# Optimization experiments

Hardware: AMD Instinct MI355X
Metric: run time of the kernel (lower is better)

Reference implementation:

```python
import jax, jax.numpy as jnp
import numpy as np

B, N, IN_DIM, HID = 16, 2048, 128, 128
EPS = 1e-5


def _layer(x, W, b, g, beta):
    # x: (B, N, d_in) -> (B, N, HID)
    h = jnp.einsum('bnd,dh->bnh', x, W) + b
    mu = jnp.mean(h, axis=-1, keepdims=True)
    var = jnp.mean((h - mu) ** 2, axis=-1, keepdims=True)
    h = (h - mu) * jax.lax.rsqrt(var + EPS) * g + beta
    return jax.nn.relu(h)


def setup_inputs() -> dict:
    key = jax.random.key(0)
    ks = jax.random.split(key, 8)
    x = jax.random.normal(ks[0], (B, N, IN_DIM), dtype=jnp.float32)
    adj = jax.random.uniform(ks[1], (B, N, N), dtype=jnp.float32)
    inp = {'x': x, 'adj': adj}
    dims = [IN_DIM, HID, HID]
    for i in range(3):
        d_in = dims[i]
        scale = 1.0 / np.sqrt(d_in)
        inp[f'W{i}'] = jax.random.uniform(ks[2 + i], (d_in, HID), dtype=jnp.float32, minval=-scale, maxval=scale)
        inp[f'b{i}'] = jax.random.uniform(ks[5 + i], (HID,), dtype=jnp.float32, minval=-scale, maxval=scale)
        inp[f'g{i}'] = jnp.ones((HID,), dtype=jnp.float32)
        inp[f'be{i}'] = jnp.zeros((HID,), dtype=jnp.float32)
    return inp


def reference(x, adj, W0, b0, g0, be0, W1, b1, g1, be1, W2, b2, g2, be2):
    params = [(W0, b0, g0, be0), (W1, b1, g1, be1), (W2, b2, g2, be2)]
    h = x
    for (W, b, g, beta) in params:
        h_agg = jnp.einsum('bnm,bmd->bnd', adj, h)  # dense adjacency aggregation
        h = _layer(h_agg, W, b, g, beta)
    return h
```

## Files before the change

### kernel.cpp

```cpp
#include <hip/hip_runtime.h>
#include <hip/hip_bf16.h>

typedef __bf16 bf16;
typedef __bf16 bf16x8 __attribute__((ext_vector_type(8)));
typedef float  f32x4  __attribute__((ext_vector_type(4)));

static constexpr int NB  = 16;
static constexpr int NN  = 2048;
static constexpr int HID = 128;

__device__ __forceinline__ void gload_lds16(const bf16* g, bf16* l) {
    __builtin_amdgcn_global_load_lds(
        (const __attribute__((address_space(1))) unsigned int*)g,
        (__attribute__((address_space(3))) unsigned int*)l, 16, 0, 0);
}
__device__ __forceinline__ void memfence() { asm volatile("" ::: "memory"); }


__global__ __launch_bounds__(256) void prep_wt(const float* __restrict__ W0,
                                               const float* __restrict__ W1,
                                               const float* __restrict__ W2,
                                               bf16* __restrict__ WTg) {
    int l = blockIdx.x;
    const float* W = (l == 0) ? W0 : (l == 1) ? W1 : W2;
    bf16* out = WTg + l * 16384;
    int tid = threadIdx.x;
#pragma unroll
    for (int i = 0; i < 8; ++i) {
        int p = i * 256 + tid;
        int n = p >> 4, half = (p >> 3) & 1, cs = p & 7;
        int kc = cs ^ (n & 7);
        int kbase = half * 64 + kc * 8;
        bf16x8 o;
#pragma unroll
        for (int r = 0; r < 8; ++r) o[r] = (bf16)W[(kbase + r) * 128 + n];
        *(bf16x8*)(out + p * 8) = o;
    }
}

__global__ __launch_bounds__(256) void prep_xt(const float* __restrict__ x,
                                               bf16* __restrict__ xTt) {
    __shared__ bf16 T[128 * 136];
    const int blk = blockIdx.x;
    const int b = blk >> 4, node0 = (blk & 15) * 128;
    const int tid = threadIdx.x;
    const float* xb = x + ((size_t)b * NN + node0) * HID;
#pragma unroll
    for (int i = 0; i < 64; ++i) {
        int idx = i * 256 + tid;
        int node = idx >> 7, hid = idx & 127;
        T[hid * 136 + node] = (bf16)xb[(size_t)node * HID + hid];
    }
    __syncthreads();
#pragma unroll
    for (int i = 0; i < 8; ++i) {
        int p = i * 256 + tid;
        int half = p >> 10, p1 = p & 1023;
        int n = p1 >> 3, cs = p1 & 7, c = cs ^ (n & 7), m = half * 64 + c * 8;
        *(bf16x8*)(xTt + ((size_t)b * 32 + (node0 >> 6) + half) * 8192 + p1 * 8)
            = *(const bf16x8*)(T + n * 136 + m);
    }
}

template<int AMODE, bool FINAL>
__global__ __launch_bounds__(512, 2) void fused_layer(
        const float* __restrict__ Af, bf16* __restrict__ adjT,
        const bf16* __restrict__ Bt, const bf16* __restrict__ WTg,
        const float* __restrict__ bias, const float* __restrict__ gam,
        const float* __restrict__ bet, bf16* __restrict__ hOut,
        float* __restrict__ outF) {
    __shared__ __align__(16) bf16 lds[49152];
    bf16* WTl = lds + 32768;

    const int tid = threadIdx.x, wave = tid >> 6, lane = tid & 63;
    const int c0 = lane & 15, q = lane >> 4;
    const int blk = blockIdx.x, xcd = blk & 7, jj = blk >> 3;
    const int b = xcd * 2 + (jj & 1);
    const int mtile = jj >> 1, m0 = mtile * 128;
    const int wm = wave >> 1, wn = wave & 1;

    const bf16* Btb = Bt + (size_t)b * 32 * 8192;
    bf16* Atl = adjT + ((size_t)b * 16 + mtile) * 32 * 8192;

    f32x4 acc[2][4] = {};

#pragma unroll
    for (int j = 0; j < 4; ++j) {
        int cb = j * 512 + wave * 64;
        gload_lds16(WTg + (size_t)(cb + lane) * 8, WTl + cb * 8);
    }

    auto stageA2 = [&](int buf, int kk) {
#pragma unroll
        for (int j = 0; j < 2; ++j) {
            int cb = j * 512 + wave * 64;
            gload_lds16(Atl + (size_t)kk * 8192 + (size_t)(cb + lane) * 8,
                        lds + buf * 16384 + cb * 8);
        }
    };
    auto stageB2 = [&](int buf, int kk) {
#pragma unroll
        for (int j = 0; j < 2; ++j) {
            int cb = j * 512 + wave * 64;
            gload_lds16(Btb + (size_t)kk * 8192 + (size_t)(cb + lane) * 8,
                        lds + buf * 16384 + 8192 + cb * 8);
        }
    };
    auto compute = [&](int buf) {
        const bf16* As = lds + buf * 16384;
        const bf16* Bs = As + 8192;
#pragma unroll
        for (int ks = 0; ks < 2; ++ks) {
            bf16x8 af[2], bf_[4];
#pragma unroll
            for (int mt = 0; mt < 2; ++mt) {
                int row = wm * 32 + mt * 16 + c0;
                int cb = (ks * 4 + q) ^ (row & 7);
                af[mt] = *(const bf16x8*)(As + row * 64 + cb * 8);
            }
#pragma unroll
            for (int nt = 0; nt < 4; ++nt) {
                int row = wn * 64 + nt * 16 + c0;
                int cb = (ks * 4 + q) ^ (row & 7);
                bf_[nt] = *(const bf16x8*)(Bs + row * 64 + cb * 8);
            }
#pragma unroll
            for (int mt = 0; mt < 2; ++mt)
#pragma unroll
                for (int nt = 0; nt < 4; ++nt)
                    acc[mt][nt] = __builtin_amdgcn_mfma_f32_16x16x32_bf16(
                        af[mt], bf_[nt], acc[mt][nt], 0, 0, 0);
        }
    };

    if constexpr (AMODE == 1) {
        int grow[2], gcb[2];
#pragma unroll
        for (int j = 0; j < 2; ++j) {
            int gi = j * 512 + tid;
            grow[j] = gi >> 3; gcb[j] = gi & 7;
        }
        f32x4 va[2], vb[2];
        auto loadA = [&](int kk) {
#pragma unroll
            for (int j = 0; j < 2; ++j) {
                const float* s = Af + (size_t)b * NN * NN
                               + (size_t)(m0 + grow[j]) * NN + kk * 64 + gcb[j] * 8;
                va[j] = *(const f32x4*)s;
                vb[j] = *(const f32x4*)(s + 4);
            }
        };
        auto writeA = [&](int buf, int kk) {
#pragma unroll
            for (int j = 0; j < 2; ++j) {
                bf16x8 o = {(bf16)va[j].x, (bf16)va[j].y, (bf16)va[j].z, (bf16)va[j].w,
                            (bf16)vb[j].x, (bf16)vb[j].y, (bf16)vb[j].z, (bf16)vb[j].w};
                int ch = grow[j] * 8 + (gcb[j] ^ (grow[j] & 7));
                *(bf16x8*)(lds + buf * 16384 + ch * 8) = o;
                *(bf16x8*)(Atl + (size_t)kk * 8192 + ch * 8) = o;
            }
        };
        loadA(0); stageB2(0, 0); writeA(0, 0);
        __syncthreads();
        int cur = 0;
        for (int kk = 0; kk < 32; ++kk) {
            if (kk < 31) { loadA(kk + 1); stageB2(cur ^ 1, kk + 1); }
            compute(cur);
            if (kk < 31) writeA(cur ^ 1, kk + 1);
            __syncthreads();
            cur ^= 1;
        }
    } else {
        stageA2(0, 0); stageB2(0, 0);
        stageA2(1, 1); stageB2(1, 1);
#pragma unroll 1
        for (int kk = 0; kk < 32; ++kk) {
            if (kk < 31) asm volatile("s_waitcnt vmcnt(4)" ::: "memory");
            else         asm volatile("s_waitcnt vmcnt(0)" ::: "memory");
            __builtin_amdgcn_s_barrier();
            memfence();
            compute(kk & 1);
            memfence();
            __builtin_amdgcn_s_barrier();
            if (kk < 30) { stageA2(kk & 1, kk + 2); stageB2(kk & 1, kk + 2); }
        }
        __syncthreads();
    }

    bf16* G = lds;
#pragma unroll
    for (int mt = 0; mt < 2; ++mt)
#pragma unroll
        for (int r = 0; r < 4; ++r) {
            int row = wm * 32 + mt * 16 + q * 4 + r;
#pragma unroll
            for (int nt = 0; nt < 4; ++nt) {
                int col = wn * 64 + nt * 16 + c0;
                G[row * 136 + col] = (bf16)acc[mt][nt][r];
            }
        }
    __syncthreads();

    f32x4 a2[8] = {};
    {
        const int gr = wave * 16 + c0;
#pragma unroll
        for (int ks = 0; ks < 4; ++ks) {
            bf16x8 af = *(const bf16x8*)(G + gr * 136 + ks * 32 + q * 8);
#pragma unroll
            for (int nt = 0; nt < 8; ++nt) {
                int n = nt * 16 + c0;
                int ch = n * 16 + (ks >> 1) * 8 + ((((ks & 1) << 2) | q) ^ (n & 7));
                bf16x8 bw = *(const bf16x8*)(WTl + ch * 8);
                a2[nt] = __builtin_amdgcn_mfma_f32_16x16x32_bf16(af, bw, a2[nt], 0, 0, 0);
            }
        }
    }

    float bv[8], gv[8], ev[8];
#pragma unroll
    for (int nt = 0; nt < 8; ++nt) {
        int n = nt * 16 + c0;
        bv[nt] = bias[n]; gv[nt] = gam[n]; ev[nt] = bet[n];
    }
    bf16* Cs = lds;
    if constexpr (!FINAL) __syncthreads();
#pragma unroll
    for (int r = 0; r < 4; ++r) {
        float v[8], s1 = 0.f, s2 = 0.f;
#pragma unroll
        for (int nt = 0; nt < 8; ++nt) {
            float xv = a2[nt][r] + bv[nt];
            v[nt] = xv; s1 += xv; s2 += xv * xv;
        }
#pragma unroll
        for (int off = 1; off < 16; off <<= 1) {
            s1 += __shfl_xor(s1, off);
            s2 += __shfl_xor(s2, off);
        }
        float mu = s1 * (1.f / 128.f);
        float var = s2 * (1.f / 128.f) - mu * mu;
        float rs = rsqrtf(var + 1e-5f);
        int row = wave * 16 + q * 4 + r;
        if constexpr (FINAL) {
            size_t ro = ((size_t)b * NN + m0 + row) * HID;
#pragma unroll
            for (int nt = 0; nt < 8; ++nt) {
                float o = fmaxf((v[nt] - mu) * rs * gv[nt] + ev[nt], 0.f);
                outF[ro + nt * 16 + c0] = o;
            }
        } else {
#pragma unroll
            for (int nt = 0; nt < 8; ++nt) {
                float o = fmaxf((v[nt] - mu) * rs * gv[nt] + ev[nt], 0.f);
                Cs[(nt * 16 + c0) * 136 + row] = (bf16)o;
            }
        }
    }
    if constexpr (!FINAL) {
        __syncthreads();
#pragma unroll
        for (int i = 0; i < 4; ++i) {
            int p = i * 512 + tid;
            int half = p >> 10, p1 = p & 1023;
            int n = p1 >> 3, cs = p1 & 7, c = cs ^ (n & 7), m = half * 64 + c * 8;
            *(bf16x8*)(hOut + ((size_t)b * 32 + mtile * 2 + half) * 8192 + p1 * 8)
                = *(const bf16x8*)(Cs + n * 136 + m);
        }
    }
}

extern "C" void kernel_launch(void* const* d_in, const int* in_sizes, int n_in,
                              void* d_out, int out_size, void* d_ws, size_t ws_size,
                              hipStream_t stream) {
    const float* x   = (const float*)d_in[0];
    const float* adj = (const float*)d_in[1];
    const float* W[3]  = {(const float*)d_in[2],  (const float*)d_in[6],  (const float*)d_in[10]};
    const float* bb[3] = {(const float*)d_in[3],  (const float*)d_in[7],  (const float*)d_in[11]};
    const float* gg[3] = {(const float*)d_in[4],  (const float*)d_in[8],  (const float*)d_in[12]};
    const float* be[3] = {(const float*)d_in[5],  (const float*)d_in[9],  (const float*)d_in[13]};

    char* ws = (char*)d_ws;
    size_t off = 0;
    auto alloc = [&](size_t bytes) {
        char* p = ws + off; off = (off + bytes + 255) & ~(size_t)255; return p;
    };
    bf16* WTg  = (bf16*)alloc((size_t)3 * 16384 * 2);
    bf16* xTt  = (bf16*)alloc((size_t)NB * 32 * 8192 * 2);
    bf16* hT0  = (bf16*)alloc((size_t)NB * 32 * 8192 * 2);
    bf16* hT1  = (bf16*)alloc((size_t)NB * 32 * 8192 * 2);
    bf16* adjT = (bf16*)alloc((size_t)NB * 16 * 32 * 8192 * 2);

    float* outF = (float*)d_out;

    prep_wt<<<3, 256, 0, stream>>>(W[0], W[1], W[2], WTg);
    prep_xt<<<256, 256, 0, stream>>>(x, xTt);

    fused_layer<1, false><<<256, 512, 0, stream>>>(adj, adjT, xTt, WTg,
                                                   bb[0], gg[0], be[0], hT0, nullptr);
    fused_layer<2, false><<<256, 512, 0, stream>>>(adj, adjT, hT0, WTg + 16384,
                                                   bb[1], gg[1], be[1], hT1, nullptr);
    fused_layer<2, true ><<<256, 512, 0, stream>>>(adj, adjT, hT1, WTg + 2 * 16384,
                                                   bb[2], gg[2], be[2], nullptr, outF);
}
```

Measured before the change: 494.7 us.

## Retile fused GNN layer to 64-row blocks with 4-stage register-fed A pipeline

Changes the fused aggregation+linear+layernorm kernel from 128-row tiles with 512 threads to 64-row tiles with 256 threads and 512 blocks. Each wave now loads its own adjacency rows straight into registers (fp32 converted in-register on layer 1, bf16 cache reused after that) instead of staging A through LDS. The B tiles are staged through a 4-deep LDS ring with vmcnt-based waits and a single barrier per step. The goal is better latency hiding on the memory-bound adjacency stream, more blocks resident per CU, and no LDS traffic for A. The cost is a changed adjT layout, more register pressure, and W being loaded late into LDS after the main loop.

```diff
diff --git a/kernel.cpp b/kernel.cpp
--- a/kernel.cpp
+++ b/kernel.cpp
@@ -14,7 +14,8 @@
         (const __attribute__((address_space(1))) unsigned int*)g,
         (__attribute__((address_space(3))) unsigned int*)l, 16, 0, 0);
 }
-__device__ __forceinline__ void memfence() { asm volatile("" ::: "memory"); }
+
+#define WAITV(n) asm volatile("s_waitcnt vmcnt(" #n ")" ::: "memory")
 
 
 __global__ __launch_bounds__(256) void prep_wt(const float* __restrict__ W0,
@@ -63,142 +64,124 @@
 }
 
 template<int AMODE, bool FINAL>
-__global__ __launch_bounds__(512, 2) void fused_layer(
+__global__ __launch_bounds__(256, 2) void fused64(
         const float* __restrict__ Af, bf16* __restrict__ adjT,
         const bf16* __restrict__ Bt, const bf16* __restrict__ WTg,
         const float* __restrict__ bias, const float* __restrict__ gam,
         const float* __restrict__ bet, bf16* __restrict__ hOut,
         float* __restrict__ outF) {
-    __shared__ __align__(16) bf16 lds[49152];
-    bf16* WTl = lds + 32768;
+    __shared__ __align__(16) bf16 lds[32768];
 
     const int tid = threadIdx.x, wave = tid >> 6, lane = tid & 63;
     const int c0 = lane & 15, q = lane >> 4;
     const int blk = blockIdx.x, xcd = blk & 7, jj = blk >> 3;
     const int b = xcd * 2 + (jj & 1);
-    const int mtile = jj >> 1, m0 = mtile * 128;
-    const int wm = wave >> 1, wn = wave & 1;
+    const int mt = jj >> 1, m0 = mt * 64;
 
     const bf16* Btb = Bt + (size_t)b * 32 * 8192;
-    bf16* Atl = adjT + ((size_t)b * 16 + mtile) * 32 * 8192;
-
-    f32x4 acc[2][4] = {};
-
-#pragma unroll
-    for (int j = 0; j < 4; ++j) {
-        int cb = j * 512 + wave * 64;
-        gload_lds16(WTg + (size_t)(cb + lane) * 8, WTl + cb * 8);
-    }
-
-    auto stageA2 = [&](int buf, int kk) {
-#pragma unroll
-        for (int j = 0; j < 2; ++j) {
-            int cb = j * 512 + wave * 64;
-            gload_lds16(Atl + (size_t)kk * 8192 + (size_t)(cb + lane) * 8,
-                        lds + buf * 16384 + cb * 8);
-        }
-    };
-    auto stageB2 = [&](int buf, int kk) {
-#pragma unroll
-        for (int j = 0; j < 2; ++j) {
-            int cb = j * 512 + wave * 64;
-            gload_lds16(Btb + (size_t)kk * 8192 + (size_t)(cb + lane) * 8,
-                        lds + buf * 16384 + 8192 + cb * 8);
-        }
-    };
-    auto compute = [&](int buf) {
-        const bf16* As = lds + buf * 16384;
-        const bf16* Bs = As + 8192;
-#pragma unroll
-        for (int ks = 0; ks < 2; ++ks) {
-            bf16x8 af[2], bf_[4];
-#pragma unroll
-            for (int mt = 0; mt < 2; ++mt) {
-                int row = wm * 32 + mt * 16 + c0;
-                int cb = (ks * 4 + q) ^ (row & 7);
-                af[mt] = *(const bf16x8*)(As + row * 64 + cb * 8);
-            }
-#pragma unroll
-            for (int nt = 0; nt < 4; ++nt) {
-                int row = wn * 64 + nt * 16 + c0;
-                int cb = (ks * 4 + q) ^ (row & 7);
-                bf_[nt] = *(const bf16x8*)(Bs + row * 64 + cb * 8);
-            }
-#pragma unroll
-            for (int mt = 0; mt < 2; ++mt)
-#pragma unroll
-                for (int nt = 0; nt < 4; ++nt)
-                    acc[mt][nt] = __builtin_amdgcn_mfma_f32_16x16x32_bf16(
-                        af[mt], bf_[nt], acc[mt][nt], 0, 0, 0);
-        }
-    };
-
-    if constexpr (AMODE == 1) {
-        int grow[2], gcb[2];
-#pragma unroll
-        for (int j = 0; j < 2; ++j) {
-            int gi = j * 512 + tid;
-            grow[j] = gi >> 3; gcb[j] = gi & 7;
-        }
-        f32x4 va[2], vb[2];
-        auto loadA = [&](int kk) {
-#pragma unroll
-            for (int j = 0; j < 2; ++j) {
-                const float* s = Af + (size_t)b * NN * NN
-                               + (size_t)(m0 + grow[j]) * NN + kk * 64 + gcb[j] * 8;
-                va[j] = *(const f32x4*)s;
-                vb[j] = *(const f32x4*)(s + 4);
-            }
-        };
-        auto writeA = [&](int buf, int kk) {
-#pragma unroll
-            for (int j = 0; j < 2; ++j) {
-                bf16x8 o = {(bf16)va[j].x, (bf16)va[j].y, (bf16)va[j].z, (bf16)va[j].w,
-                            (bf16)vb[j].x, (bf16)vb[j].y, (bf16)vb[j].z, (bf16)vb[j].w};
-                int ch = grow[j] * 8 + (gcb[j] ^ (grow[j] & 7));
-                *(bf16x8*)(lds + buf * 16384 + ch * 8) = o;
-                *(bf16x8*)(Atl + (size_t)kk * 8192 + ch * 8) = o;
-            }
-        };
-        loadA(0); stageB2(0, 0); writeA(0, 0);
-        __syncthreads();
-        int cur = 0;
-        for (int kk = 0; kk < 32; ++kk) {
-            if (kk < 31) { loadA(kk + 1); stageB2(cur ^ 1, kk + 1); }
-            compute(cur);
-            if (kk < 31) writeA(cur ^ 1, kk + 1);
-            __syncthreads();
-            cur ^= 1;
-        }
-    } else {
-        stageA2(0, 0); stageB2(0, 0);
-        stageA2(1, 1); stageB2(1, 1);
+    bf16* Atl = adjT + ((size_t)b * 32 + mt) * (size_t)32 * 4096;
+    const float* Aln = Af + (size_t)b * NN * NN
+                     + (size_t)(m0 + wave * 16 + c0) * NN + q * 8;
+    const int fofs = wave * 128 + lane;
+
+    f32x4 acc[8] = {};
+    bf16x8 aA[4][2];
+    f32x4  aF[4][2][2];
+
+#define LOADA(S, KK) do {                                                     \
+    if constexpr (AMODE == 1) {                                               \
+        _Pragma("unroll") for (int ks = 0; ks < 2; ++ks) {                    \
+            const float* s_ = Aln + (KK) * 64 + ks * 32;                      \
+            aF[S][ks][0] = *(const f32x4*)s_;                                 \
+            aF[S][ks][1] = *(const f32x4*)(s_ + 4);                           \
+        }                                                                     \
+    } else {                                                                  \
+        _Pragma("unroll") for (int ks = 0; ks < 2; ++ks)                      \
+            aA[S][ks] = *(const bf16x8*)(Atl + (size_t)(KK) * 4096            \
+                                         + (fofs + ks * 64) * 8);             \
+    } } while (0)
+
+#define STAGEB(S, KK) do {                                                    \
+    _Pragma("unroll") for (int j = 0; j < 4; ++j) {                           \
+        int cb = j * 256 + wave * 64;                                         \
+        gload_lds16(Btb + (size_t)(KK) * 8192 + (size_t)(cb + lane) * 8,      \
+                    lds + (S) * 8192 + cb * 8);                               \
+    } } while (0)
+
+#define COMP(S, KK) do {                                                      \
+    bf16x8 af_[2];                                                            \
+    if constexpr (AMODE == 1) {                                               \
+        _Pragma("unroll") for (int ks = 0; ks < 2; ++ks) {                    \
+            f32x4 lo = aF[S][ks][0], hi = aF[S][ks][1];                       \
+            bf16x8 o = {(bf16)lo.x, (bf16)lo.y, (bf16)lo.z, (bf16)lo.w,       \
+                        (bf16)hi.x, (bf16)hi.y, (bf16)hi.z, (bf16)hi.w};      \
+            af_[ks] = o;                                                      \
+            *(bf16x8*)(Atl + (size_t)(KK) * 4096 + (fofs + ks * 64) * 8) = o; \
+        }                                                                     \
+    } else { af_[0] = aA[S][0]; af_[1] = aA[S][1]; }                          \
+    const bf16* Bs_ = lds + (S) * 8192;                                       \
+    _Pragma("unroll") for (int ks = 0; ks < 2; ++ks)                          \
+        _Pragma("unroll") for (int nt = 0; nt < 8; ++nt) {                    \
+            int row = nt * 16 + c0, cb = (ks * 4 + q) ^ (row & 7);            \
+            bf16x8 bw = *(const bf16x8*)(Bs_ + row * 64 + cb * 8);            \
+            acc[nt] = __builtin_amdgcn_mfma_f32_16x16x32_bf16(                \
+                af_[ks], bw, acc[nt], 0, 0, 0);                               \
+        } } while (0)
+
+    LOADA(0, 0); STAGEB(0, 0);
+    LOADA(1, 1); STAGEB(1, 1);
+    LOADA(2, 2); STAGEB(2, 2);
+
+#define ITERU(U, KB)                                                          \
+    { if constexpr (AMODE == 1) WAITV(20); else WAITV(12);                    \
+      __builtin_amdgcn_s_barrier();                                           \
+      COMP(U, (KB) + (U));                                                    \
+      LOADA(((U) + 3) & 3, (KB) + (U) + 3);                                   \
+      STAGEB(((U) + 3) & 3, (KB) + (U) + 3); }
+
 #pragma unroll 1
-        for (int kk = 0; kk < 32; ++kk) {
-            if (kk < 31) asm volatile("s_waitcnt vmcnt(4)" ::: "memory");
-            else         asm volatile("s_waitcnt vmcnt(0)" ::: "memory");
-            __builtin_amdgcn_s_barrier();
-            memfence();
-            compute(kk & 1);
-            memfence();
-            __builtin_amdgcn_s_barrier();
-            if (kk < 30) { stageA2(kk & 1, kk + 2); stageB2(kk & 1, kk + 2); }
-        }
-        __syncthreads();
-    }
-
+    for (int t = 0; t < 7; ++t) {
+        const int kb = t * 4;
+        ITERU(0, kb) ITERU(1, kb) ITERU(2, kb) ITERU(3, kb)
+    }
+    if constexpr (AMODE == 1) WAITV(20); else WAITV(12);
+    __builtin_amdgcn_s_barrier();
+    COMP(0, 28);
+    LOADA(3, 31); STAGEB(3, 31);
+
+    if constexpr (AMODE == 1) WAITV(20); else WAITV(12);
+    __builtin_amdgcn_s_barrier();
+    COMP(1, 29);
+
+    if constexpr (AMODE == 1) WAITV(12); else WAITV(6);
+    __builtin_amdgcn_s_barrier();
+    COMP(2, 30);
+
+    if constexpr (AMODE == 1) WAITV(4); else WAITV(0);
+    __builtin_amdgcn_s_barrier();
+    COMP(3, 31);
+
+#undef ITERU
+#undef COMP
+#undef STAGEB
+#undef LOADA
+
+    __syncthreads();
+
+#pragma unroll
+    for (int j = 0; j < 8; ++j) {
+        int cb = j * 256 + wave * 64;
+        gload_lds16(WTg + (size_t)(cb + lane) * 8, lds + 16384 + cb * 8);
+    }
     bf16* G = lds;
 #pragma unroll
-    for (int mt = 0; mt < 2; ++mt)
+    for (int nt = 0; nt < 8; ++nt)
 #pragma unroll
         for (int r = 0; r < 4; ++r) {
-            int row = wm * 32 + mt * 16 + q * 4 + r;
-#pragma unroll
-            for (int nt = 0; nt < 4; ++nt) {
-                int col = wn * 64 + nt * 16 + c0;
-                G[row * 136 + col] = (bf16)acc[mt][nt][r];
-            }
-        }
+            int row = wave * 16 + q * 4 + r;
+            G[row * 136 + nt * 16 + c0] = (bf16)acc[nt][r];
+        }
+    WAITV(0);
     __syncthreads();
 
     f32x4 a2[8] = {};
@@ -211,8 +194,8 @@
             for (int nt = 0; nt < 8; ++nt) {
                 int n = nt * 16 + c0;
                 int ch = n * 16 + (ks >> 1) * 8 + ((((ks & 1) << 2) | q) ^ (n & 7));
-                bf16x8 bw = *(const bf16x8*)(WTl + ch * 8);
-                a2[nt] = __builtin_amdgcn_mfma_f32_16x16x32_bf16(af, bw, a2[nt], 0, 0, 0);
+                a2[nt] = __builtin_amdgcn_mfma_f32_16x16x32_bf16(
+                    af, *(const bf16x8*)(lds + 16384 + ch * 8), a2[nt], 0, 0, 0);
             }
         }
     }
@@ -253,7 +236,7 @@
 #pragma unroll
             for (int nt = 0; nt < 8; ++nt) {
                 float o = fmaxf((v[nt] - mu) * rs * gv[nt] + ev[nt], 0.f);
-                Cs[(nt * 16 + c0) * 136 + row] = (bf16)o;
+                Cs[(nt * 16 + c0) * 72 + row] = (bf16)o;
             }
         }
     }
@@ -261,11 +244,10 @@
         __syncthreads();
 #pragma unroll
         for (int i = 0; i < 4; ++i) {
-            int p = i * 512 + tid;
-            int half = p >> 10, p1 = p & 1023;
-            int n = p1 >> 3, cs = p1 & 7, c = cs ^ (n & 7), m = half * 64 + c * 8;
-            *(bf16x8*)(hOut + ((size_t)b * 32 + mtile * 2 + half) * 8192 + p1 * 8)
-                = *(const bf16x8*)(Cs + n * 136 + m);
+            int p1 = i * 256 + tid;
+            int n = p1 >> 3, cs = p1 & 7, c = cs ^ (n & 7), m = c * 8;
+            *(bf16x8*)(hOut + ((size_t)b * 32 + mt) * 8192 + p1 * 8)
+                = *(const bf16x8*)(Cs + n * 72 + m);
         }
     }
 }
@@ -289,17 +271,17 @@
     bf16* xTt  = (bf16*)alloc((size_t)NB * 32 * 8192 * 2);
     bf16* hT0  = (bf16*)alloc((size_t)NB * 32 * 8192 * 2);
     bf16* hT1  = (bf16*)alloc((size_t)NB * 32 * 8192 * 2);
-    bf16* adjT = (bf16*)alloc((size_t)NB * 16 * 32 * 8192 * 2);
+    bf16* adjT = (bf16*)alloc((size_t)NB * 32 * 32 * 4096 * 2);
 
     float* outF = (float*)d_out;
 
     prep_wt<<<3, 256, 0, stream>>>(W[0], W[1], W[2], WTg);
     prep_xt<<<256, 256, 0, stream>>>(x, xTt);
 
-    fused_layer<1, false><<<256, 512, 0, stream>>>(adj, adjT, xTt, WTg,
-                                                   bb[0], gg[0], be[0], hT0, nullptr);
-    fused_layer<2, false><<<256, 512, 0, stream>>>(adj, adjT, hT0, WTg + 16384,
-                                                   bb[1], gg[1], be[1], hT1, nullptr);
-    fused_layer<2, true ><<<256, 512, 0, stream>>>(adj, adjT, hT1, WTg + 2 * 16384,
-                                                   bb[2], gg[2], be[2], nullptr, outF);
-}
+    fused64<1, false><<<512, 256, 0, stream>>>(adj, adjT, xTt, WTg,
+                                               bb[0], gg[0], be[0], hT0, nullptr);
+    fused64<2, false><<<512, 256, 0, stream>>>(adj, adjT, hT0, WTg + 16384,
+                                               bb[1], gg[1], be[1], hT1, nullptr);
+    fused64<2, true ><<<512, 256, 0, stream>>>(adj, adjT, hT1, WTg + 2 * 16384,
+                                               bb[2], gg[2], be[2], nullptr, outF);
+}
```

Result: slower. 533.2 us (+7.8%).

## Merge three layer kernels into one persistent kernel with grid barriers

Applied to the files above, without the earlier changes.

The three per-layer launches become a single persistent kernel that runs each layer in turn, separated by software grid-wide barriers built on atomic counters in workspace. The counters are zeroed by the weight-prep kernel. The aim is to remove the launch gaps and tail effects between layers. It relies on all 256 blocks being co-resident, which holds at 2 blocks per CU on 256 CUs, and it adds spin-wait cost at each barrier.

```diff
diff --git a/kernel.cpp b/kernel.cpp
--- a/kernel.cpp
+++ b/kernel.cpp
@@ -14,17 +14,32 @@
         (const __attribute__((address_space(1))) unsigned int*)g,
         (__attribute__((address_space(3))) unsigned int*)l, 16, 0, 0);
 }
-__device__ __forceinline__ void memfence() { asm volatile("" ::: "memory"); }
+
+#define WAITV(n) asm volatile("s_waitcnt vmcnt(" #n ")" ::: "memory")
+
+__device__ __forceinline__ void gbar(unsigned* cnt, unsigned nb) {
+    __syncthreads();
+    if (threadIdx.x == 0) {
+        __threadfence();
+        __hip_atomic_fetch_add(cnt, 1u, __ATOMIC_ACQ_REL, __HIP_MEMORY_SCOPE_AGENT);
+        while (__hip_atomic_load(cnt, __ATOMIC_ACQUIRE, __HIP_MEMORY_SCOPE_AGENT) < nb)
+            __builtin_amdgcn_s_sleep(2);
+        __threadfence();
+    }
+    __syncthreads();
+}
 
 
 __global__ __launch_bounds__(256) void prep_wt(const float* __restrict__ W0,
                                                const float* __restrict__ W1,
                                                const float* __restrict__ W2,
-                                               bf16* __restrict__ WTg) {
+                                               bf16* __restrict__ WTg,
+                                               unsigned* __restrict__ sync) {
     int l = blockIdx.x;
+    int tid = threadIdx.x;
+    if (l == 0 && tid < 64) sync[tid] = 0u;
     const float* W = (l == 0) ? W0 : (l == 1) ? W1 : W2;
     bf16* out = WTg + l * 16384;
-    int tid = threadIdx.x;
 #pragma unroll
     for (int i = 0; i < 8; ++i) {
         int p = i * 256 + tid;
@@ -63,24 +78,21 @@
 }
 
 template<int AMODE, bool FINAL>
-__global__ __launch_bounds__(512, 2) void fused_layer(
-        const float* __restrict__ Af, bf16* __restrict__ adjT,
-        const bf16* __restrict__ Bt, const bf16* __restrict__ WTg,
+__device__ __forceinline__ void layer_run(
+        bf16* lds,
+        const float* __restrict__ Afb,
+        bf16* __restrict__ Atl,
+        const bf16* __restrict__ Btb,
+        const bf16* __restrict__ WTg,
         const float* __restrict__ bias, const float* __restrict__ gam,
-        const float* __restrict__ bet, bf16* __restrict__ hOut,
-        float* __restrict__ outF) {
-    __shared__ __align__(16) bf16 lds[49152];
+        const float* __restrict__ bet,
+        bf16* __restrict__ hOut, float* __restrict__ outF,
+        int b, int mtile, int m0) {
     bf16* WTl = lds + 32768;
 
     const int tid = threadIdx.x, wave = tid >> 6, lane = tid & 63;
     const int c0 = lane & 15, q = lane >> 4;
-    const int blk = blockIdx.x, xcd = blk & 7, jj = blk >> 3;
-    const int b = xcd * 2 + (jj & 1);
-    const int mtile = jj >> 1, m0 = mtile * 128;
     const int wm = wave >> 1, wn = wave & 1;
-
-    const bf16* Btb = Bt + (size_t)b * 32 * 8192;
-    bf16* Atl = adjT + ((size_t)b * 16 + mtile) * 32 * 8192;
 
     f32x4 acc[2][4] = {};
 
@@ -144,8 +156,7 @@
         auto loadA = [&](int kk) {
 #pragma unroll
             for (int j = 0; j < 2; ++j) {
-                const float* s = Af + (size_t)b * NN * NN
-                               + (size_t)(m0 + grow[j]) * NN + kk * 64 + gcb[j] * 8;
+                const float* s = Afb + (size_t)(m0 + grow[j]) * NN + kk * 64 + gcb[j] * 8;
                 va[j] = *(const f32x4*)s;
                 vb[j] = *(const f32x4*)(s + 4);
             }
@@ -175,12 +186,12 @@
         stageA2(1, 1); stageB2(1, 1);
 #pragma unroll 1
         for (int kk = 0; kk < 32; ++kk) {
-            if (kk < 31) asm volatile("s_waitcnt vmcnt(4)" ::: "memory");
-            else         asm volatile("s_waitcnt vmcnt(0)" ::: "memory");
+            if (kk < 31) WAITV(4);
+            else         WAITV(0);
             __builtin_amdgcn_s_barrier();
-            memfence();
+            asm volatile("" ::: "memory");
             compute(kk & 1);
-            memfence();
+            asm volatile("" ::: "memory");
             __builtin_amdgcn_s_barrier();
             if (kk < 30) { stageA2(kk & 1, kk + 2); stageB2(kk & 1, kk + 2); }
         }
@@ -268,6 +279,33 @@
                 = *(const bf16x8*)(Cs + n * 136 + m);
         }
     }
+}
+
+__global__ __launch_bounds__(512, 2) void mega(
+        const float* __restrict__ adj, bf16* __restrict__ adjT,
+        const bf16* __restrict__ xTt, const bf16* __restrict__ WTg,
+        const float* __restrict__ b0, const float* __restrict__ g0, const float* __restrict__ e0,
+        const float* __restrict__ b1, const float* __restrict__ g1, const float* __restrict__ e1,
+        const float* __restrict__ b2, const float* __restrict__ g2, const float* __restrict__ e2,
+        bf16* __restrict__ hT0, bf16* __restrict__ hT1,
+        float* __restrict__ outF, unsigned* __restrict__ sync) {
+    __shared__ __align__(16) bf16 lds[49152];
+
+    const int blk = blockIdx.x, xcd = blk & 7, jj = blk >> 3;
+    const int b = xcd * 2 + (jj & 1);
+    const int mtile = jj >> 1, m0 = mtile * 128;
+
+    const float* Afb = adj + (size_t)b * NN * NN;
+    bf16* Atl = adjT + ((size_t)b * 16 + mtile) * (size_t)32 * 8192;
+
+    layer_run<1, false>(lds, Afb, Atl, xTt + (size_t)b * 32 * 8192, WTg,
+                        b0, g0, e0, hT0, nullptr, b, mtile, m0);
+    gbar(sync + 0, 256);
+    layer_run<2, false>(lds, Afb, Atl, hT0 + (size_t)b * 32 * 8192, WTg + 16384,
+                        b1, g1, e1, hT1, nullptr, b, mtile, m0);
+    gbar(sync + 1, 256);
+    layer_run<2, true >(lds, Afb, Atl, hT1 + (size_t)b * 32 * 8192, WTg + 2 * 16384,
+                        b2, g2, e2, nullptr, outF, b, mtile, m0);
 }
 
 extern "C" void kernel_launch(void* const* d_in, const int* in_sizes, int n_in,
@@ -285,6 +323,7 @@
     auto alloc = [&](size_t bytes) {
         char* p = ws + off; off = (off + bytes + 255) & ~(size_t)255; return p;
     };
+    unsigned* sync = (unsigned*)alloc(256);
     bf16* WTg  = (bf16*)alloc((size_t)3 * 16384 * 2);
     bf16* xTt  = (bf16*)alloc((size_t)NB * 32 * 8192 * 2);
     bf16* hT0  = (bf16*)alloc((size_t)NB * 32 * 8192 * 2);
@@ -293,13 +332,12 @@
 
     float* outF = (float*)d_out;
 
-    prep_wt<<<3, 256, 0, stream>>>(W[0], W[1], W[2], WTg);
+    prep_wt<<<3, 256, 0, stream>>>(W[0], W[1], W[2], WTg, sync);
     prep_xt<<<256, 256, 0, stream>>>(x, xTt);
 
-    fused_layer<1, false><<<256, 512, 0, stream>>>(adj, adjT, xTt, WTg,
-                                                   bb[0], gg[0], be[0], hT0, nullptr);
-    fused_layer<2, false><<<256, 512, 0, stream>>>(adj, adjT, hT0, WTg + 16384,
-                                                   bb[1], gg[1], be[1], hT1, nullptr);
-    fused_layer<2, true ><<<256, 512, 0, stream>>>(adj, adjT, hT1, WTg + 2 * 16384,
-                                                   bb[2], gg[2], be[2], nullptr, outF);
-}
+    mega<<<256, 512, 0, stream>>>(adj, adjT, xTt, WTg,
+                                  bb[0], gg[0], be[0],
+                                  bb[1], gg[1], be[1],
+                                  bb[2], gg[2], be[2],
+                                  hT0, hT1, outF, sync);
+}
```

New measurement: 556.8 us. 12.6% more time.

## Shrink row tile to 64 with 4-wave blocks and triple-buffered pipeline

Applied to the files above, without the earlier changes.

The fused layer kernel now uses 64-row output tiles with 256-thread blocks, doubling the grid to 512 blocks. The K-loop moves from double to triple buffering with a single barrier per step. The first layer's fp32 adjacency load and bf16 convert now run inside that pipeline instead of a separate synchronous loop, and the W matrix is read straight from global memory rather than staged in LDS. The aim is better CU fill and latency hiding. In exchange each block rereads the full B operand for only half as many rows, and the W reads in the second GEMM go to global memory.

```diff
diff --git a/kernel.cpp b/kernel.cpp
--- a/kernel.cpp
+++ b/kernel.cpp
@@ -14,7 +14,8 @@
         (const __attribute__((address_space(1))) unsigned int*)g,
         (__attribute__((address_space(3))) unsigned int*)l, 16, 0, 0);
 }
-__device__ __forceinline__ void memfence() { asm volatile("" ::: "memory"); }
+
+#define WAITV(n) asm volatile("s_waitcnt vmcnt(" #n ")" ::: "memory")
 
 
 __global__ __launch_bounds__(256) void prep_wt(const float* __restrict__ W0,
@@ -63,141 +64,119 @@
 }
 
 template<int AMODE, bool FINAL>
-__global__ __launch_bounds__(512, 2) void fused_layer(
+__global__ __launch_bounds__(256, 2) void layer64(
         const float* __restrict__ Af, bf16* __restrict__ adjT,
         const bf16* __restrict__ Bt, const bf16* __restrict__ WTg,
         const float* __restrict__ bias, const float* __restrict__ gam,
         const float* __restrict__ bet, bf16* __restrict__ hOut,
         float* __restrict__ outF) {
-    __shared__ __align__(16) bf16 lds[49152];
-    bf16* WTl = lds + 32768;
+    __shared__ __align__(16) bf16 lds[36864];
 
     const int tid = threadIdx.x, wave = tid >> 6, lane = tid & 63;
     const int c0 = lane & 15, q = lane >> 4;
     const int blk = blockIdx.x, xcd = blk & 7, jj = blk >> 3;
     const int b = xcd * 2 + (jj & 1);
-    const int mtile = jj >> 1, m0 = mtile * 128;
-    const int wm = wave >> 1, wn = wave & 1;
+    const int mt = jj >> 1, m0 = mt * 64;
 
     const bf16* Btb = Bt + (size_t)b * 32 * 8192;
-    bf16* Atl = adjT + ((size_t)b * 16 + mtile) * 32 * 8192;
-
-    f32x4 acc[2][4] = {};
-
-#pragma unroll
-    for (int j = 0; j < 4; ++j) {
-        int cb = j * 512 + wave * 64;
-        gload_lds16(WTg + (size_t)(cb + lane) * 8, WTl + cb * 8);
-    }
-
-    auto stageA2 = [&](int buf, int kk) {
+    bf16* Atl = adjT + ((size_t)b * 32 + mt) * (size_t)(32 * 4096);
+    const float* Afb = Af + (size_t)b * NN * NN + (size_t)m0 * NN;
+
+    f32x4 acc[8] = {};
+
+    auto stageA = [&](int buf, int kk) {
 #pragma unroll
         for (int j = 0; j < 2; ++j) {
-            int cb = j * 512 + wave * 64;
-            gload_lds16(Atl + (size_t)kk * 8192 + (size_t)(cb + lane) * 8,
-                        lds + buf * 16384 + cb * 8);
-        }
-    };
-    auto stageB2 = [&](int buf, int kk) {
+            int cb = j * 256 + wave * 64;
+            gload_lds16(Atl + (size_t)kk * 4096 + (size_t)(cb + lane) * 8,
+                        lds + buf * 12288 + cb * 8);
+        }
+    };
+    auto stageB = [&](int buf, int kk) {
+#pragma unroll
+        for (int j = 0; j < 4; ++j) {
+            int cb = j * 256 + wave * 64;
+            gload_lds16(Btb + (size_t)kk * 8192 + (size_t)(cb + lane) * 8,
+                        lds + buf * 12288 + 4096 + cb * 8);
+        }
+    };
+
+    int g_row[2], g_cb[2];
+#pragma unroll
+    for (int j = 0; j < 2; ++j) {
+        int gi = j * 256 + tid;
+        g_row[j] = gi >> 3; g_cb[j] = gi & 7;
+    }
+    f32x4 va[2], vb[2];
+    auto loadA = [&](int kk) {
 #pragma unroll
         for (int j = 0; j < 2; ++j) {
-            int cb = j * 512 + wave * 64;
-            gload_lds16(Btb + (size_t)kk * 8192 + (size_t)(cb + lane) * 8,
-                        lds + buf * 16384 + 8192 + cb * 8);
+            const float* s = Afb + (size_t)g_row[j] * NN + kk * 64 + g_cb[j] * 8;
+            va[j] = *(const f32x4*)s;
+            vb[j] = *(const f32x4*)(s + 4);
+        }
+    };
+    auto writeA = [&](int buf, int kk) {
+#pragma unroll
+        for (int j = 0; j < 2; ++j) {
+            bf16x8 o = {(bf16)va[j].x, (bf16)va[j].y, (bf16)va[j].z, (bf16)va[j].w,
+                        (bf16)vb[j].x, (bf16)vb[j].y, (bf16)vb[j].z, (bf16)vb[j].w};
+            int ch = g_row[j] * 8 + (g_cb[j] ^ (g_row[j] & 7));
+            *(bf16x8*)(lds + buf * 12288 + ch * 8) = o;
+            *(bf16x8*)(Atl + (size_t)kk * 4096 + ch * 8) = o;
         }
     };
     auto compute = [&](int buf) {
-        const bf16* As = lds + buf * 16384;
-        const bf16* Bs = As + 8192;
+        const bf16* As = lds + buf * 12288;
+        const bf16* Bs = As + 4096;
 #pragma unroll
         for (int ks = 0; ks < 2; ++ks) {
-            bf16x8 af[2], bf_[4];
-#pragma unroll
-            for (int mt = 0; mt < 2; ++mt) {
-                int row = wm * 32 + mt * 16 + c0;
-                int cb = (ks * 4 + q) ^ (row & 7);
-                af[mt] = *(const bf16x8*)(As + row * 64 + cb * 8);
-            }
-#pragma unroll
-            for (int nt = 0; nt < 4; ++nt) {
-                int row = wn * 64 + nt * 16 + c0;
-                int cb = (ks * 4 + q) ^ (row & 7);
-                bf_[nt] = *(const bf16x8*)(Bs + row * 64 + cb * 8);
-            }
-#pragma unroll
-            for (int mt = 0; mt < 2; ++mt)
-#pragma unroll
-                for (int nt = 0; nt < 4; ++nt)
-                    acc[mt][nt] = __builtin_amdgcn_mfma_f32_16x16x32_bf16(
-                        af[mt], bf_[nt], acc[mt][nt], 0, 0, 0);
+            int kb = ks * 4 + q;
+            int ar = wave * 16 + c0;
+            bf16x8 af = *(const bf16x8*)(As + ar * 64 + (kb ^ (ar & 7)) * 8);
+#pragma unroll
+            for (int nt = 0; nt < 8; ++nt) {
+                int br = nt * 16 + c0;
+                bf16x8 bw = *(const bf16x8*)(Bs + br * 64 + (kb ^ (br & 7)) * 8);
+                acc[nt] = __builtin_amdgcn_mfma_f32_16x16x32_bf16(af, bw, acc[nt], 0, 0, 0);
+            }
         }
     };
 
     if constexpr (AMODE == 1) {
-        int grow[2], gcb[2];
-#pragma unroll
-        for (int j = 0; j < 2; ++j) {
-            int gi = j * 512 + tid;
-            grow[j] = gi >> 3; gcb[j] = gi & 7;
-        }
-        f32x4 va[2], vb[2];
-        auto loadA = [&](int kk) {
-#pragma unroll
-            for (int j = 0; j < 2; ++j) {
-                const float* s = Af + (size_t)b * NN * NN
-                               + (size_t)(m0 + grow[j]) * NN + kk * 64 + gcb[j] * 8;
-                va[j] = *(const f32x4*)s;
-                vb[j] = *(const f32x4*)(s + 4);
-            }
-        };
-        auto writeA = [&](int buf, int kk) {
-#pragma unroll
-            for (int j = 0; j < 2; ++j) {
-                bf16x8 o = {(bf16)va[j].x, (bf16)va[j].y, (bf16)va[j].z, (bf16)va[j].w,
-                            (bf16)vb[j].x, (bf16)vb[j].y, (bf16)vb[j].z, (bf16)vb[j].w};
-                int ch = grow[j] * 8 + (gcb[j] ^ (grow[j] & 7));
-                *(bf16x8*)(lds + buf * 16384 + ch * 8) = o;
-                *(bf16x8*)(Atl + (size_t)kk * 8192 + ch * 8) = o;
-            }
-        };
-        loadA(0); stageB2(0, 0); writeA(0, 0);
-        __syncthreads();
-        int cur = 0;
-        for (int kk = 0; kk < 32; ++kk) {
-            if (kk < 31) { loadA(kk + 1); stageB2(cur ^ 1, kk + 1); }
-            compute(cur);
-            if (kk < 31) writeA(cur ^ 1, kk + 1);
-            __syncthreads();
-            cur ^= 1;
-        }
+        loadA(0); writeA(0, 0); stageB(0, 0);
+        loadA(1); writeA(1, 1); stageB(1, 1);
     } else {
-        stageA2(0, 0); stageB2(0, 0);
-        stageA2(1, 1); stageB2(1, 1);
+        stageA(0, 0); stageB(0, 0);
+        stageA(1, 1); stageB(1, 1);
+    }
+
+    int bufk = 0;
 #pragma unroll 1
-        for (int kk = 0; kk < 32; ++kk) {
-            if (kk < 31) asm volatile("s_waitcnt vmcnt(4)" ::: "memory");
-            else         asm volatile("s_waitcnt vmcnt(0)" ::: "memory");
-            __builtin_amdgcn_s_barrier();
-            memfence();
-            compute(kk & 1);
-            memfence();
-            __builtin_amdgcn_s_barrier();
-            if (kk < 30) { stageA2(kk & 1, kk + 2); stageB2(kk & 1, kk + 2); }
-        }
-        __syncthreads();
-    }
+    for (int kk = 0; kk < 32; ++kk) {
+        if (kk < 31) WAITV(6);
+        else         WAITV(0);
+        __builtin_amdgcn_s_barrier();
+        const int b2 = bufk ? bufk - 1 : 2;
+        if constexpr (AMODE == 1) {
+            if (kk < 30) loadA(kk + 2);
+            compute(bufk);
+            if (kk < 30) { writeA(b2, kk + 2); stageB(b2, kk + 2); }
+        } else {
+            compute(bufk);
+            if (kk < 30) { stageA(b2, kk + 2); stageB(b2, kk + 2); }
+        }
+        bufk = (bufk == 2) ? 0 : bufk + 1;
+    }
+    __syncthreads();
 
     bf16* G = lds;
 #pragma unroll
-    for (int mt = 0; mt < 2; ++mt)
+    for (int nt = 0; nt < 8; ++nt)
 #pragma unroll
         for (int r = 0; r < 4; ++r) {
-            int row = wm * 32 + mt * 16 + q * 4 + r;
-#pragma unroll
-            for (int nt = 0; nt < 4; ++nt) {
-                int col = wn * 64 + nt * 16 + c0;
-                G[row * 136 + col] = (bf16)acc[mt][nt][r];
-            }
+            int row = wave * 16 + q * 4 + r;
+            G[row * 136 + nt * 16 + c0] = (bf16)acc[nt][r];
         }
     __syncthreads();
 
@@ -211,7 +190,7 @@
             for (int nt = 0; nt < 8; ++nt) {
                 int n = nt * 16 + c0;
                 int ch = n * 16 + (ks >> 1) * 8 + ((((ks & 1) << 2) | q) ^ (n & 7));
-                bf16x8 bw = *(const bf16x8*)(WTl + ch * 8);
+                bf16x8 bw = *(const bf16x8*)(WTg + (size_t)ch * 8);
                 a2[nt] = __builtin_amdgcn_mfma_f32_16x16x32_bf16(af, bw, a2[nt], 0, 0, 0);
             }
         }
@@ -253,7 +232,7 @@
 #pragma unroll
             for (int nt = 0; nt < 8; ++nt) {
                 float o = fmaxf((v[nt] - mu) * rs * gv[nt] + ev[nt], 0.f);
-                Cs[(nt * 16 + c0) * 136 + row] = (bf16)o;
+                Cs[(nt * 16 + c0) * 72 + row] = (bf16)o;
             }
         }
     }
@@ -261,11 +240,10 @@
         __syncthreads();
 #pragma unroll
         for (int i = 0; i < 4; ++i) {
-            int p = i * 512 + tid;
-            int half = p >> 10, p1 = p & 1023;
-            int n = p1 >> 3, cs = p1 & 7, c = cs ^ (n & 7), m = half * 64 + c * 8;
-            *(bf16x8*)(hOut + ((size_t)b * 32 + mtile * 2 + half) * 8192 + p1 * 8)
-                = *(const bf16x8*)(Cs + n * 136 + m);
+            int p1 = i * 256 + tid;
+            int n = p1 >> 3, cs = p1 & 7, c = cs ^ (n & 7), m = c * 8;
+            *(bf16x8*)(hOut + ((size_t)b * 32 + mt) * 8192 + p1 * 8)
+                = *(const bf16x8*)(Cs + n * 72 + m);
         }
     }
 }
@@ -289,17 +267,17 @@
     bf16* xTt  = (bf16*)alloc((size_t)NB * 32 * 8192 * 2);
     bf16* hT0  = (bf16*)alloc((size_t)NB * 32 * 8192 * 2);
     bf16* hT1  = (bf16*)alloc((size_t)NB * 32 * 8192 * 2);
-    bf16* adjT = (bf16*)alloc((size_t)NB * 16 * 32 * 8192 * 2);
+    bf16* adjT = (bf16*)alloc((size_t)NB * 32 * 32 * 4096 * 2);
 
     float* outF = (float*)d_out;
 
     prep_wt<<<3, 256, 0, stream>>>(W[0], W[1], W[2], WTg);
     prep_xt<<<256, 256, 0, stream>>>(x, xTt);
 
-    fused_layer<1, false><<<256, 512, 0, stream>>>(adj, adjT, xTt, WTg,
-                                                   bb[0], gg[0], be[0], hT0, nullptr);
-    fused_layer<2, false><<<256, 512, 0, stream>>>(adj, adjT, hT0, WTg + 16384,
-                                                   bb[1], gg[1], be[1], hT1, nullptr);
-    fused_layer<2, true ><<<256, 512, 0, stream>>>(adj, adjT, hT1, WTg + 2 * 16384,
-                                                   bb[2], gg[2], be[2], nullptr, outF);
-}
+    layer64<1, false><<<512, 256, 0, stream>>>(adj, adjT, xTt, WTg,
+                                               bb[0], gg[0], be[0], hT0, nullptr);
+    layer64<2, false><<<512, 256, 0, stream>>>(adj, adjT, hT0, WTg + 16384,
+                                               bb[1], gg[1], be[1], hT1, nullptr);
+    layer64<2, true ><<<512, 256, 0, stream>>>(adj, adjT, hT1, WTg + 2 * 16384,
+                                               bb[2], gg[2], be[2], nullptr, outF);
+}
```

Result: slower. 513.9 us (+3.9%).
